# Performance work log

Measured on AMD Instinct MI355X. Metric: run time of the kernel, lower is better.

Reference implementation:

```python
import jax, jax.numpy as jnp
import numpy as np

B, C, D, H, W = 2, 128, 32, 64, 64  # ch_in=128, shurink=0 -> Cs = ch_out = C
Cs = C


def setup_inputs() -> dict:
    key = jax.random.key(0)
    ks = jax.random.split(key, 9)
    std = 1.0 / np.sqrt(C).astype(np.float32)
    x = jax.random.normal(ks[0], (B, C, D, H, W), jnp.float32)
    Wk = jax.random.normal(ks[1], (Cs, C), jnp.float32) * std
    bk = jax.random.normal(ks[2], (Cs,), jnp.float32) * std
    Wq = jax.random.normal(ks[3], (Cs, C), jnp.float32) * std
    bq = jax.random.normal(ks[4], (Cs,), jnp.float32) * std
    Wv = jax.random.normal(ks[5], (Cs, C), jnp.float32) * std
    bv = jax.random.normal(ks[6], (Cs,), jnp.float32) * std
    Wo = jax.random.normal(ks[7], (C, Cs), jnp.float32) * (1.0 / np.sqrt(Cs).astype(np.float32))
    bo = jax.random.normal(ks[8], (C,), jnp.float32) * std
    return {"x": x, "Wk": Wk, "bk": bk, "Wq": Wq, "bq": bq, "Wv": Wv, "bv": bv, "Wo": Wo, "bo": bo}


def reference(x, Wk, bk, Wq, bq, Wv, bv, Wo, bo):
    # 1x1x1 Conv3d == per-voxel linear over channels
    def proj(Wt, bt):
        return jnp.einsum('bcdhw,oc->bodhw', x, Wt) + bt[None, :, None, None, None]

    K = proj(Wk, bk)  # [B,Cs,D,H,W]
    Q = proj(Wq, bq)
    V = proj(Wv, bv)

    scale = 1.0 / jnp.sqrt(jnp.asarray(Cs, x.dtype))
    # per-pixel depth attention: scores[b,h,w,i,j] = sum_c K[b,c,i,h,w] * Q[b,c,j,h,w]
    scores = jnp.einsum('bcihw,bcjhw->bhwij', K, Q) * scale
    # torch softmax dim=1 on [N,D,D] == key-position axis i (axis=-2 here)
    A = jax.nn.softmax(scores, axis=-2)
    # a[b,c,j,h,w] = sum_i V[b,c,i,h,w] * A[b,h,w,i,j]  (== bmm(V, A))
    a = jnp.einsum('bcihw,bhwij->bcjhw', V, A)
    out = jnp.einsum('bcjhw,oc->bojhw', a, Wo) + bo[None, :, None, None, None]
    return x + out  # atten_factor = 1
```

## Files before the change

### kernel.cpp

```cpp
#include <hip/hip_runtime.h>

typedef _Float16 f16x8 __attribute__((ext_vector_type(8)));
typedef _Float16 f16x4 __attribute__((ext_vector_type(4)));
typedef float    f32x4 __attribute__((ext_vector_type(4)));

#define MFMA(a,b,c) __builtin_amdgcn_mfma_f32_16x16x32_f16((a),(b),(c),0,0,0)


__global__ __launch_bounds__(128) void prep_kernel(
    const float* __restrict__ Wk, const float* __restrict__ bk,
    const float* __restrict__ Wq, const float* __restrict__ bq,
    const float* __restrict__ Wv, const float* __restrict__ bv,
    const float* __restrict__ Wo, const float* __restrict__ bo,
    _Float16* __restrict__ wh, float* __restrict__ bf) {
  __shared__ float shK[128], shO[128];
  const int o = blockIdx.x;
  const int c = threadIdx.x;
  const float scale = 0.08838834764831844f;
  shK[c] = Wk[c*128 + o];
  shO[c] = Wo[o*128 + c];
  __syncthreads();
  float aM = 0.f, aV = 0.f, tK = 0.f, bV = 0.f;
  for (int m = 0; m < 128; ++m) {
    aM += shK[m] * Wq[m*128 + c];
    aV += shO[m] * Wv[m*128 + c];
    tK += shK[m] * bq[m];
    bV += shO[m] * bv[m];
  }
  wh[o*128 + c]         = (_Float16)(aM * scale);
  wh[16384 + o*128 + c] = (_Float16)aV;
  if (c == 0) { bf[o] = tK * scale; bf[128 + o] = bV + bo[o]; }
}

__global__ __launch_bounds__(256) void transpose_kernel(
    const float* __restrict__ x, _Float16* __restrict__ Xg) {
  __shared__ _Float16 Lt[64 * 132];
  const int bid = blockIdx.x;
  const int h = bid & 63, d = (bid >> 6) & 31, b = bid >> 11;
  const int tid = threadIdx.x;
  const int wq = tid & 15, cr = tid >> 4;
  const size_t rbase = (size_t)b*16777216u + (size_t)d*4096 + h*64;
#pragma unroll
  for (int pass = 0; pass < 2; ++pass) {
    const int base_c = pass*64 + cr*4;
    f32x4 v[4];
#pragma unroll
    for (int r = 0; r < 4; ++r)
      v[r] = *(const f32x4*)(x + rbase + (size_t)(base_c + r)*131072 + wq*4);
#pragma unroll
    for (int p = 0; p < 4; ++p) {
      f16x4 t;
#pragma unroll
      for (int r = 0; r < 4; ++r) t[r] = (_Float16)v[r][p];
      *(f16x4*)(Lt + (wq*4 + p)*132 + base_c) = t;
    }
  }
  __syncthreads();
  const int gbase = (b*64 + h)*8;
#pragma unroll
  for (int i = 0; i < 4; ++i) {
    const int idx = tid + i*256;
    const int w = idx >> 4, ck = (idx & 15) * 8;
    const f16x8 v = *(const f16x8*)(Lt + w*132 + ck);
    *(f16x8*)(Xg + (size_t)(gbase + (w>>3))*32768 + (d*8 + (w&7))*128 + ck) = v;
  }
}

__device__ __forceinline__ f16x4 cvt4(f32x4 v, f32x4 b) {
  f16x4 r;
  r[0] = (_Float16)(v[0] + b[0]); r[1] = (_Float16)(v[1] + b[1]);
  r[2] = (_Float16)(v[2] + b[2]); r[3] = (_Float16)(v[3] + b[3]);
  return r;
}
__device__ __forceinline__ f16x4 cvt4z(f32x4 v) {
  f16x4 r;
  r[0] = (_Float16)v[0]; r[1] = (_Float16)v[1];
  r[2] = (_Float16)v[2]; r[3] = (_Float16)v[3];
  return r;
}

__device__ __forceinline__ int xsw(int row, int col ) {
  return ((row << 8) | (col << 1)) ^ (((row ^ (row >> 3) ^ (row >> 5)) & 7) << 4);
}

__global__ __launch_bounds__(1024, 4) void attn_kernel(
    const _Float16* __restrict__ Xg, const _Float16* __restrict__ wh,
    const float* __restrict__ bfp, float* __restrict__ out) {
  __shared__ __align__(16) char lds[151552];
  char* XtB = lds;
  char* YtB = lds + 65536;
  _Float16* At = (_Float16*)(lds + 131072);

  const int tid  = threadIdx.x;
  const int lane = tid & 63;
  const int wv   = tid >> 6;
  const int quad = lane >> 4;
  const int l15  = lane & 15;

  const int bid = blockIdx.x;
  const int g = (bid & ~15) | ((bid & 7) << 1) | ((bid >> 3) & 1);
  const int b   = g >> 9;
  const int rem = g & 511;
  const int h   = rem >> 3;
  const int wg  = rem & 7;
  const size_t pbase = (size_t)b * 16777216u + (size_t)(h*64 + wg*8);
  const f32x4 zz = {0.f, 0.f, 0.f, 0.f};

  const int mi = wv & 7, ni = wv >> 3;
  f16x8 wm[4];
#pragma unroll
  for (int kk = 0; kk < 4; ++kk)
    wm[kk] = *(const f16x8*)(wh + (mi*16 + l15)*128 + kk*32 + quad*8);
  const f32x4 t4 = *(const f32x4*)(bfp + mi*16 + quad*4);

  {
    const _Float16* src = Xg + (size_t)g * 32768;
#pragma unroll
    for (int i = 0; i < 4; ++i) {
      const int idx = tid + i*1024;
      const int row = idx >> 4, ck = (idx & 15) * 8;
      const f16x8 v = *(const f16x8*)(src + row*128 + ck);
      *(f16x8*)(XtB + xsw(row, ck)) = v;
    }
  }
  __syncthreads();

  {
    f32x4 aY[8] = {zz, zz, zz, zz, zz, zz, zz, zz};
#pragma unroll
    for (int kk = 0; kk < 4; ++kk) {
      const int co = kk*32 + quad*8;
#pragma unroll
      for (int nt = 0; nt < 8; ++nt) {
        const f16x8 bfv = *(const f16x8*)(XtB + xsw(ni*128 + nt*16 + l15, co));
        aY[nt] = MFMA(wm[kk], bfv, aY[nt]);
      }
    }
#pragma unroll
    for (int nt = 0; nt < 8; ++nt)
      *(f16x4*)(YtB + xsw(ni*128 + nt*16 + l15, mi*16 + quad*4)) = cvt4(aY[nt], t4);
  }
  __syncthreads();

  {
    const int p = wv & 7, tj = wv >> 3;
    f32x4 aS[2] = {zz, zz};
#pragma unroll
    for (int kk = 0; kk < 4; ++kk) {
      const int co = kk*32 + quad*8;
      const f16x8 by = *(const f16x8*)(YtB + xsw((tj*16 + l15)*8 + p, co));
#pragma unroll
      for (int ti = 0; ti < 2; ++ti) {
        const f16x8 ak = *(const f16x8*)(XtB + xsw((ti*16 + l15)*8 + p, co));
        aS[ti] = MFMA(ak, by, aS[ti]);
      }
    }
    float mx = aS[0][0];
#pragma unroll
    for (int r = 1; r < 4; ++r) mx = fmaxf(mx, aS[0][r]);
#pragma unroll
    for (int r = 0; r < 4; ++r) mx = fmaxf(mx, aS[1][r]);
    mx = fmaxf(mx, __shfl_xor(mx, 16));
    mx = fmaxf(mx, __shfl_xor(mx, 32));
    float e[2][4];
    float den = 0.f;
#pragma unroll
    for (int ti = 0; ti < 2; ++ti)
#pragma unroll
      for (int r = 0; r < 4; ++r) { e[ti][r] = __expf(aS[ti][r] - mx); den += e[ti][r]; }
    den += __shfl_xor(den, 16);
    den += __shfl_xor(den, 32);
    const float rr = 1.0f / den;
#pragma unroll
    for (int ti = 0; ti < 2; ++ti) {
      f16x4 av;
#pragma unroll
      for (int r = 0; r < 4; ++r) av[r] = (_Float16)(e[ti][r] * rr);
      *(f16x4*)(At + (p*32 + tj*16 + l15)*40 + ti*16 + quad*4) = av;
    }
  }
  __syncthreads();

  f16x8 wp[4];
  {
#pragma unroll
    for (int kk = 0; kk < 4; ++kk)
      wp[kk] = *(const f16x8*)(wh + 16384 + (mi*16 + l15)*128 + kk*32 + quad*8);
    const int p = wv & 7, mg = wv >> 3;
    f16x8 bA[2];
#pragma unroll
    for (int tj = 0; tj < 2; ++tj)
      bA[tj] = *(const f16x8*)(At + (p*32 + tj*16 + l15)*40 + quad*8);
#pragma unroll
    for (int t2 = 0; t2 < 4; ++t2) {
      const int ms = mg*4 + t2;
      f16x8 ax;
#pragma unroll
      for (int jj = 0; jj < 8; ++jj)
        ax[jj] = *(const _Float16*)(XtB + xsw((quad*8 + jj)*8 + p, ms*16 + l15));
#pragma unroll
      for (int tj = 0; tj < 2; ++tj) {
        const f32x4 aU = MFMA(ax, bA[tj], zz);
        *(f16x4*)(YtB + xsw((tj*16 + l15)*8 + p, ms*16 + quad*4)) = cvt4z(aU);
      }
    }
  }
  __syncthreads();

  {
    const int oi = wv & 7, mg6 = wv >> 3;
    f32x4 acc[8] = {zz, zz, zz, zz, zz, zz, zz, zz};
#pragma unroll
    for (int kk = 0; kk < 4; ++kk) {
      const int co = kk*32 + quad*8;
#pragma unroll
      for (int mt = 0; mt < 8; ++mt) {
        const f16x8 av = *(const f16x8*)(YtB + xsw((mg6*8 + mt)*16 + l15, co));
        acc[mt] = MFMA(av, wp[kk], acc[mt]);
      }
    }
    const int o = oi*16 + l15;
    const float bb = bfp[128 + o];
    float* outp = out + pbase + (size_t)o*131072;
#pragma unroll
    for (int mt = 0; mt < 8; ++mt) {
      const int vox0 = (mg6*8 + mt)*16 + quad*4;
      const int d = vox0 >> 3;
      f32x4 v;
#pragma unroll
      for (int r = 0; r < 4; ++r)
        v[r] = acc[mt][r] + bb +
               (float)*(const _Float16*)(XtB + xsw(vox0 + r, o));
      *(f32x4*)(outp + (size_t)d*4096 + (vox0 & 7)) = v;
    }
  }
}

extern "C" void kernel_launch(void* const* d_in, const int* in_sizes, int n_in,
                              void* d_out, int out_size, void* d_ws, size_t ws_size,
                              hipStream_t stream) {
  const float* x  = (const float*)d_in[0];
  const float* Wk = (const float*)d_in[1];
  const float* bk = (const float*)d_in[2];
  const float* Wq = (const float*)d_in[3];
  const float* bq = (const float*)d_in[4];
  const float* Wv = (const float*)d_in[5];
  const float* bv = (const float*)d_in[6];
  const float* Wo = (const float*)d_in[7];
  const float* bo = (const float*)d_in[8];
  float* out = (float*)d_out;
  _Float16* wh = (_Float16*)d_ws;
  float* bf = (float*)((char*)d_ws + 65536);
  _Float16* Xg = (_Float16*)((char*)d_ws + 131072);

  prep_kernel<<<dim3(128), dim3(128), 0, stream>>>(Wk, bk, Wq, bq, Wv, bv, Wo, bo, wh, bf);
  transpose_kernel<<<dim3(4096), dim3(256), 0, stream>>>(x, Xg);
  attn_kernel<<<dim3(1024), dim3(1024), 0, stream>>>(Xg, wh, bf, out);
}
```

Before: 343.6 us.

## Make attention kernel persistent with register prefetch of next tile

The attention kernel now launches 256 blocks, each looping over 4 tiles instead of one tile per block. Weights and bias stay loaded in registers across iterations. The next tile's input is prefetched from global memory into registers while the current tile's output projection and store run, hiding load latency. In exchange, grid parallelism drops to one block per CU, which removes inter-block overlap, and the extra prefetch registers add pressure.

```diff
diff --git a/kernel.cpp b/kernel.cpp
--- a/kernel.cpp
+++ b/kernel.cpp
@@ -96,15 +96,11 @@
   const int wv   = tid >> 6;
   const int quad = lane >> 4;
   const int l15  = lane & 15;
-
-  const int bid = blockIdx.x;
-  const int g = (bid & ~15) | ((bid & 7) << 1) | ((bid >> 3) & 1);
-  const int b   = g >> 9;
-  const int rem = g & 511;
-  const int h   = rem >> 3;
-  const int wg  = rem & 7;
-  const size_t pbase = (size_t)b * 16777216u + (size_t)(h*64 + wg*8);
+  const int bid  = blockIdx.x;
   const f32x4 zz = {0.f, 0.f, 0.f, 0.f};
+
+  const int rowi[4] = { (tid)>>4, (tid+1024)>>4, (tid+2048)>>4, (tid+3072)>>4 };
+  const int cki [4] = { (tid&15)*8, (tid&15)*8, (tid&15)*8, (tid&15)*8 };
 
   const int mi = wv & 7, ni = wv >> 3;
   f16x8 wm[4];
@@ -112,127 +108,144 @@
   for (int kk = 0; kk < 4; ++kk)
     wm[kk] = *(const f16x8*)(wh + (mi*16 + l15)*128 + kk*32 + quad*8);
   const f32x4 t4 = *(const f32x4*)(bfp + mi*16 + quad*4);
-
-  {
-    const _Float16* src = Xg + (size_t)g * 32768;
-#pragma unroll
-    for (int i = 0; i < 4; ++i) {
-      const int idx = tid + i*1024;
-      const int row = idx >> 4, ck = (idx & 15) * 8;
-      const f16x8 v = *(const f16x8*)(src + row*128 + ck);
-      *(f16x8*)(XtB + xsw(row, ck)) = v;
-    }
-  }
-  __syncthreads();
-
-  {
-    f32x4 aY[8] = {zz, zz, zz, zz, zz, zz, zz, zz};
-#pragma unroll
-    for (int kk = 0; kk < 4; ++kk) {
-      const int co = kk*32 + quad*8;
-#pragma unroll
-      for (int nt = 0; nt < 8; ++nt) {
-        const f16x8 bfv = *(const f16x8*)(XtB + xsw(ni*128 + nt*16 + l15, co));
-        aY[nt] = MFMA(wm[kk], bfv, aY[nt]);
-      }
-    }
-#pragma unroll
-    for (int nt = 0; nt < 8; ++nt)
-      *(f16x4*)(YtB + xsw(ni*128 + nt*16 + l15, mi*16 + quad*4)) = cvt4(aY[nt], t4);
-  }
-  __syncthreads();
-
-  {
-    const int p = wv & 7, tj = wv >> 3;
-    f32x4 aS[2] = {zz, zz};
-#pragma unroll
-    for (int kk = 0; kk < 4; ++kk) {
-      const int co = kk*32 + quad*8;
-      const f16x8 by = *(const f16x8*)(YtB + xsw((tj*16 + l15)*8 + p, co));
+  const float bb = bfp[128 + (wv & 7)*16 + l15];
+
+  int orig = bid;
+  int g = (orig & ~15) | ((orig & 7) << 1) | ((orig >> 3) & 1);
+
+  f16x8 pf[4];
+#pragma unroll
+  for (int i = 0; i < 4; ++i)
+    pf[i] = *(const f16x8*)(Xg + (size_t)g*32768 + (size_t)(tid + i*1024)*8);
+
+  for (int it = 0; it < 4; ++it) {
+    const int b   = g >> 9;
+    const int rem = g & 511;
+    const size_t pbase = (size_t)b * 16777216u
+                       + (size_t)((rem >> 3)*64 + (rem & 7)*8);
+
+#pragma unroll
+    for (int i = 0; i < 4; ++i)
+      *(f16x8*)(XtB + xsw(rowi[i], cki[i])) = pf[i];
+    __syncthreads();
+
+    {
+      f32x4 aY[8] = {zz, zz, zz, zz, zz, zz, zz, zz};
+#pragma unroll
+      for (int kk = 0; kk < 4; ++kk) {
+        const int co = kk*32 + quad*8;
+#pragma unroll
+        for (int nt = 0; nt < 8; ++nt) {
+          const f16x8 bfv = *(const f16x8*)(XtB + xsw(ni*128 + nt*16 + l15, co));
+          aY[nt] = MFMA(wm[kk], bfv, aY[nt]);
+        }
+      }
+#pragma unroll
+      for (int nt = 0; nt < 8; ++nt)
+        *(f16x4*)(YtB + xsw(ni*128 + nt*16 + l15, mi*16 + quad*4)) = cvt4(aY[nt], t4);
+    }
+    __syncthreads();
+
+    {
+      const int p = wv & 7, tj = wv >> 3;
+      f32x4 aS[2] = {zz, zz};
+#pragma unroll
+      for (int kk = 0; kk < 4; ++kk) {
+        const int co = kk*32 + quad*8;
+        const f16x8 by = *(const f16x8*)(YtB + xsw((tj*16 + l15)*8 + p, co));
+#pragma unroll
+        for (int ti = 0; ti < 2; ++ti) {
+          const f16x8 ak = *(const f16x8*)(XtB + xsw((ti*16 + l15)*8 + p, co));
+          aS[ti] = MFMA(ak, by, aS[ti]);
+        }
+      }
+      float mx = aS[0][0];
+#pragma unroll
+      for (int r = 1; r < 4; ++r) mx = fmaxf(mx, aS[0][r]);
+#pragma unroll
+      for (int r = 0; r < 4; ++r) mx = fmaxf(mx, aS[1][r]);
+      mx = fmaxf(mx, __shfl_xor(mx, 16));
+      mx = fmaxf(mx, __shfl_xor(mx, 32));
+      float e[2][4];
+      float den = 0.f;
+#pragma unroll
+      for (int ti = 0; ti < 2; ++ti)
+#pragma unroll
+        for (int r = 0; r < 4; ++r) { e[ti][r] = __expf(aS[ti][r] - mx); den += e[ti][r]; }
+      den += __shfl_xor(den, 16);
+      den += __shfl_xor(den, 32);
+      const float rr = 1.0f / den;
 #pragma unroll
       for (int ti = 0; ti < 2; ++ti) {
-        const f16x8 ak = *(const f16x8*)(XtB + xsw((ti*16 + l15)*8 + p, co));
-        aS[ti] = MFMA(ak, by, aS[ti]);
-      }
-    }
-    float mx = aS[0][0];
-#pragma unroll
-    for (int r = 1; r < 4; ++r) mx = fmaxf(mx, aS[0][r]);
-#pragma unroll
-    for (int r = 0; r < 4; ++r) mx = fmaxf(mx, aS[1][r]);
-    mx = fmaxf(mx, __shfl_xor(mx, 16));
-    mx = fmaxf(mx, __shfl_xor(mx, 32));
-    float e[2][4];
-    float den = 0.f;
-#pragma unroll
-    for (int ti = 0; ti < 2; ++ti)
-#pragma unroll
-      for (int r = 0; r < 4; ++r) { e[ti][r] = __expf(aS[ti][r] - mx); den += e[ti][r]; }
-    den += __shfl_xor(den, 16);
-    den += __shfl_xor(den, 32);
-    const float rr = 1.0f / den;
-#pragma unroll
-    for (int ti = 0; ti < 2; ++ti) {
-      f16x4 av;
-#pragma unroll
-      for (int r = 0; r < 4; ++r) av[r] = (_Float16)(e[ti][r] * rr);
-      *(f16x4*)(At + (p*32 + tj*16 + l15)*40 + ti*16 + quad*4) = av;
-    }
-  }
-  __syncthreads();
-
-  f16x8 wp[4];
-  {
-#pragma unroll
-    for (int kk = 0; kk < 4; ++kk)
-      wp[kk] = *(const f16x8*)(wh + 16384 + (mi*16 + l15)*128 + kk*32 + quad*8);
-    const int p = wv & 7, mg = wv >> 3;
-    f16x8 bA[2];
-#pragma unroll
-    for (int tj = 0; tj < 2; ++tj)
-      bA[tj] = *(const f16x8*)(At + (p*32 + tj*16 + l15)*40 + quad*8);
-#pragma unroll
-    for (int t2 = 0; t2 < 4; ++t2) {
-      const int ms = mg*4 + t2;
-      f16x8 ax;
-#pragma unroll
-      for (int jj = 0; jj < 8; ++jj)
-        ax[jj] = *(const _Float16*)(XtB + xsw((quad*8 + jj)*8 + p, ms*16 + l15));
-#pragma unroll
-      for (int tj = 0; tj < 2; ++tj) {
-        const f32x4 aU = MFMA(ax, bA[tj], zz);
-        *(f16x4*)(YtB + xsw((tj*16 + l15)*8 + p, ms*16 + quad*4)) = cvt4z(aU);
-      }
-    }
-  }
-  __syncthreads();
-
-  {
-    const int oi = wv & 7, mg6 = wv >> 3;
-    f32x4 acc[8] = {zz, zz, zz, zz, zz, zz, zz, zz};
-#pragma unroll
-    for (int kk = 0; kk < 4; ++kk) {
-      const int co = kk*32 + quad*8;
+        f16x4 av;
+#pragma unroll
+        for (int r = 0; r < 4; ++r) av[r] = (_Float16)(e[ti][r] * rr);
+        *(f16x4*)(At + (p*32 + tj*16 + l15)*40 + ti*16 + quad*4) = av;
+      }
+    }
+    __syncthreads();
+
+    f16x8 wp[4];
+    {
+#pragma unroll
+      for (int kk = 0; kk < 4; ++kk)
+        wp[kk] = *(const f16x8*)(wh + 16384 + (mi*16 + l15)*128 + kk*32 + quad*8);
+      const int p = wv & 7, mg = wv >> 3;
+      f16x8 bA[2];
+#pragma unroll
+      for (int tj = 0; tj < 2; ++tj)
+        bA[tj] = *(const f16x8*)(At + (p*32 + tj*16 + l15)*40 + quad*8);
+#pragma unroll
+      for (int t2 = 0; t2 < 4; ++t2) {
+        const int ms = mg*4 + t2;
+        f16x8 ax;
+#pragma unroll
+        for (int jj = 0; jj < 8; ++jj)
+          ax[jj] = *(const _Float16*)(XtB + xsw((quad*8 + jj)*8 + p, ms*16 + l15));
+#pragma unroll
+        for (int tj = 0; tj < 2; ++tj) {
+          const f32x4 aU = MFMA(ax, bA[tj], zz);
+          *(f16x4*)(YtB + xsw((tj*16 + l15)*8 + p, ms*16 + quad*4)) = cvt4z(aU);
+        }
+      }
+    }
+
+    if (it < 3) {
+      orig += 256;
+      g = (orig & ~15) | ((orig & 7) << 1) | ((orig >> 3) & 1);
+#pragma unroll
+      for (int i = 0; i < 4; ++i)
+        pf[i] = *(const f16x8*)(Xg + (size_t)g*32768 + (size_t)(tid + i*1024)*8);
+    }
+    __syncthreads();
+
+    {
+      const int oi = wv & 7, mg6 = wv >> 3;
+      f32x4 acc[8] = {zz, zz, zz, zz, zz, zz, zz, zz};
+#pragma unroll
+      for (int kk = 0; kk < 4; ++kk) {
+        const int co = kk*32 + quad*8;
+#pragma unroll
+        for (int mt = 0; mt < 8; ++mt) {
+          const f16x8 av = *(const f16x8*)(YtB + xsw((mg6*8 + mt)*16 + l15, co));
+          acc[mt] = MFMA(av, wp[kk], acc[mt]);
+        }
+      }
+      const int o = oi*16 + l15;
+      float* outp = out + pbase + (size_t)o*131072;
 #pragma unroll
       for (int mt = 0; mt < 8; ++mt) {
-        const f16x8 av = *(const f16x8*)(YtB + xsw((mg6*8 + mt)*16 + l15, co));
-        acc[mt] = MFMA(av, wp[kk], acc[mt]);
-      }
-    }
-    const int o = oi*16 + l15;
-    const float bb = bfp[128 + o];
-    float* outp = out + pbase + (size_t)o*131072;
-#pragma unroll
-    for (int mt = 0; mt < 8; ++mt) {
-      const int vox0 = (mg6*8 + mt)*16 + quad*4;
-      const int d = vox0 >> 3;
-      f32x4 v;
-#pragma unroll
-      for (int r = 0; r < 4; ++r)
-        v[r] = acc[mt][r] + bb +
-               (float)*(const _Float16*)(XtB + xsw(vox0 + r, o));
-      *(f32x4*)(outp + (size_t)d*4096 + (vox0 & 7)) = v;
-    }
+        const int vox0 = (mg6*8 + mt)*16 + quad*4;
+        const int d = vox0 >> 3;
+        f32x4 v;
+#pragma unroll
+        for (int r = 0; r < 4; ++r)
+          v[r] = acc[mt][r] + bb +
+                 (float)*(const _Float16*)(XtB + xsw(vox0 + r, o));
+        *(f32x4*)(outp + (size_t)d*4096 + (vox0 & 7)) = v;
+      }
+    }
+    __syncthreads();
   }
 }
 
@@ -255,5 +268,5 @@
 
   prep_kernel<<<dim3(128), dim3(128), 0, stream>>>(Wk, bk, Wq, bq, Wv, bv, Wo, bo, wh, bf);
   transpose_kernel<<<dim3(4096), dim3(256), 0, stream>>>(x, Xg);
-  attn_kernel<<<dim3(1024), dim3(1024), 0, stream>>>(Xg, wh, bf, out);
-}
+  attn_kernel<<<dim3(256), dim3(1024), 0, stream>>>(Xg, wh, bf, out);
+}
```

New measurement: 535.9 us. 1.56x slower.

## Fuse fp32-to-fp16 transpose into attention kernel, drop transpose pass

Applied to the files above, without the earlier changes.

Removes the separate transpose kernel that converted x to a voxel-major fp16 buffer in workspace. The attention kernel now loads its 8-wide w strip of x directly in fp32 (32-byte segments per channel/depth row), converts to fp16 and writes to swizzled LDS. This cuts a full extra read and write of the activation tensor and one launch. The cost is narrower, less coalesced global reads inside the main kernel and more register pressure at kernel start.

```diff
diff --git a/kernel.cpp b/kernel.cpp
--- a/kernel.cpp
+++ b/kernel.cpp
@@ -32,40 +32,6 @@
   if (c == 0) { bf[o] = tK * scale; bf[128 + o] = bV + bo[o]; }
 }
 
-__global__ __launch_bounds__(256) void transpose_kernel(
-    const float* __restrict__ x, _Float16* __restrict__ Xg) {
-  __shared__ _Float16 Lt[64 * 132];
-  const int bid = blockIdx.x;
-  const int h = bid & 63, d = (bid >> 6) & 31, b = bid >> 11;
-  const int tid = threadIdx.x;
-  const int wq = tid & 15, cr = tid >> 4;
-  const size_t rbase = (size_t)b*16777216u + (size_t)d*4096 + h*64;
-#pragma unroll
-  for (int pass = 0; pass < 2; ++pass) {
-    const int base_c = pass*64 + cr*4;
-    f32x4 v[4];
-#pragma unroll
-    for (int r = 0; r < 4; ++r)
-      v[r] = *(const f32x4*)(x + rbase + (size_t)(base_c + r)*131072 + wq*4);
-#pragma unroll
-    for (int p = 0; p < 4; ++p) {
-      f16x4 t;
-#pragma unroll
-      for (int r = 0; r < 4; ++r) t[r] = (_Float16)v[r][p];
-      *(f16x4*)(Lt + (wq*4 + p)*132 + base_c) = t;
-    }
-  }
-  __syncthreads();
-  const int gbase = (b*64 + h)*8;
-#pragma unroll
-  for (int i = 0; i < 4; ++i) {
-    const int idx = tid + i*256;
-    const int w = idx >> 4, ck = (idx & 15) * 8;
-    const f16x8 v = *(const f16x8*)(Lt + w*132 + ck);
-    *(f16x8*)(Xg + (size_t)(gbase + (w>>3))*32768 + (d*8 + (w&7))*128 + ck) = v;
-  }
-}
-
 __device__ __forceinline__ f16x4 cvt4(f32x4 v, f32x4 b) {
   f16x4 r;
   r[0] = (_Float16)(v[0] + b[0]); r[1] = (_Float16)(v[1] + b[1]);
@@ -84,7 +50,7 @@
 }
 
 __global__ __launch_bounds__(1024, 4) void attn_kernel(
-    const _Float16* __restrict__ Xg, const _Float16* __restrict__ wh,
+    const float* __restrict__ x, const _Float16* __restrict__ wh,
     const float* __restrict__ bfp, float* __restrict__ out) {
   __shared__ __align__(16) char lds[151552];
   char* XtB = lds;
@@ -106,6 +72,18 @@
   const size_t pbase = (size_t)b * 16777216u + (size_t)(h*64 + wg*8);
   const f32x4 zz = {0.f, 0.f, 0.f, 0.f};
 
+  const int c4 = tid & 31;
+  const int dd = tid >> 5;
+  f32x4 v[4][2];
+  {
+    const float* xg = x + pbase + (size_t)c4*4*131072 + (size_t)dd*4096;
+#pragma unroll
+    for (int r = 0; r < 4; ++r)
+#pragma unroll
+      for (int i = 0; i < 2; ++i)
+        v[r][i] = *(const f32x4*)(xg + (size_t)r*131072 + i*4);
+  }
+
   const int mi = wv & 7, ni = wv >> 3;
   f16x8 wm[4];
 #pragma unroll
@@ -113,16 +91,15 @@
     wm[kk] = *(const f16x8*)(wh + (mi*16 + l15)*128 + kk*32 + quad*8);
   const f32x4 t4 = *(const f32x4*)(bfp + mi*16 + quad*4);
 
-  {
-    const _Float16* src = Xg + (size_t)g * 32768;
-#pragma unroll
-    for (int i = 0; i < 4; ++i) {
-      const int idx = tid + i*1024;
-      const int row = idx >> 4, ck = (idx & 15) * 8;
-      const f16x8 v = *(const f16x8*)(src + row*128 + ck);
-      *(f16x8*)(XtB + xsw(row, ck)) = v;
-    }
-  }
+#pragma unroll
+  for (int i = 0; i < 2; ++i)
+#pragma unroll
+    for (int p = 0; p < 4; ++p) {
+      f16x4 t;
+#pragma unroll
+      for (int r = 0; r < 4; ++r) t[r] = (_Float16)v[r][i][p];
+      *(f16x4*)(XtB + xsw(dd*8 + i*4 + p, c4*4)) = t;
+    }
   __syncthreads();
 
   {
@@ -226,12 +203,12 @@
     for (int mt = 0; mt < 8; ++mt) {
       const int vox0 = (mg6*8 + mt)*16 + quad*4;
       const int d = vox0 >> 3;
-      f32x4 v;
+      f32x4 vv;
 #pragma unroll
       for (int r = 0; r < 4; ++r)
-        v[r] = acc[mt][r] + bb +
-               (float)*(const _Float16*)(XtB + xsw(vox0 + r, o));
-      *(f32x4*)(outp + (size_t)d*4096 + (vox0 & 7)) = v;
+        vv[r] = acc[mt][r] + bb +
+                (float)*(const _Float16*)(XtB + xsw(vox0 + r, o));
+      *(f32x4*)(outp + (size_t)d*4096 + (vox0 & 7)) = vv;
     }
   }
 }
@@ -251,9 +228,7 @@
   float* out = (float*)d_out;
   _Float16* wh = (_Float16*)d_ws;
   float* bf = (float*)((char*)d_ws + 65536);
-  _Float16* Xg = (_Float16*)((char*)d_ws + 131072);
 
   prep_kernel<<<dim3(128), dim3(128), 0, stream>>>(Wk, bk, Wq, bq, Wv, bv, Wo, bo, wh, bf);
-  transpose_kernel<<<dim3(4096), dim3(256), 0, stream>>>(x, Xg);
-  attn_kernel<<<dim3(1024), dim3(1024), 0, stream>>>(Xg, wh, bf, out);
-}
+  attn_kernel<<<dim3(1024), dim3(1024), 0, stream>>>(x, wh, bf, out);
+}
```

New measurement: 347.4 us. About the same (+1.1%).
